# Performance work log

Hardware: AMD Instinct MI355X
Metric: run time of the kernel (lower is better)

The kernel has to match this reference:

```python
import jax, jax.numpy as jnp
import numpy as np

N_LAYERS, D_MODEL, H, D_K, D_V, D_FF, VOCAB = 6, 512, 8, 64, 64, 2048, 32000
B, S = 4, 512
NEG_INF = -jnp.inf


def positional_encoding(seq_len, d_model):
    # Faithful to the (buggy-vs-paper) source: angle = pos / 10000**(2*i/d_model),
    # sin for even i, cos for odd i (i is the raw channel index).
    pos = jnp.arange(seq_len, dtype=jnp.float32)[:, None]
    i = jnp.arange(d_model, dtype=jnp.float32)[None, :]
    angle = pos / jnp.power(10000.0, 2.0 * i / d_model)
    return jnp.where((jnp.arange(d_model) % 2 == 0)[None, :], jnp.sin(angle), jnp.cos(angle))


def layer_norm(x, g, b, eps=1e-5):
    mu = jnp.mean(x, -1, keepdims=True)
    var = jnp.mean((x - mu) ** 2, -1, keepdims=True)
    return (x - mu) * jax.lax.rsqrt(var + eps) * g + b


def mha(q_in, k_in, v_in, wq, wk, wv, wo, q_mask, k_mask, causal):
    # wq/wk: (H, D, D_K), wv: (H, D, D_V), wo: (H*D_V, D)
    q = jnp.einsum('bsd,hdk->bhsk', q_in, wq)
    k = jnp.einsum('btd,hdk->bhtk', k_in, wk)
    v = jnp.einsum('btd,hdk->bhtk', v_in, wv)
    scores = jnp.einsum('bhsk,bhtk->bhst', q, k) / jnp.sqrt(jnp.float32(D_K))
    allowed = q_mask[:, None, :, None] & k_mask[:, None, None, :]  # (B,1,S,T)
    if causal:
        sl, tl = q_in.shape[1], k_in.shape[1]
        allowed = allowed & (jnp.arange(tl)[None, :] <= jnp.arange(sl)[:, None])[None, None]
    scores = jnp.where(allowed, scores, NEG_INF)
    attn = jax.nn.softmax(scores, axis=-1)
    out = jnp.einsum('bhst,bhtk->bshk', attn, v)  # (B,S,H,D_V)
    out = out.reshape(out.shape[0], out.shape[1], H * D_V)
    return out @ wo


def ffn(x, w1, b1, w2, b2):
    return jax.nn.relu(x @ w1 + b1) @ w2 + b2


def setup_inputs() -> dict:
    key = jax.random.key(0)
    ks = iter(jax.random.split(key, 40))
    f = lambda shape, scale: (jax.random.normal(next(ks), shape, dtype=jnp.float32) * scale)
    inp = {
        'src_tokens': jax.random.randint(next(ks), (B, S), 0, VOCAB),
        'tgt_tokens': jax.random.randint(next(ks), (B, S), 0, VOCAB),
        'src_mask': jnp.ones((B, S), dtype=bool),
        'tgt_mask': jnp.ones((B, S), dtype=bool),
        'embed': f((VOCAB, D_MODEL), 0.02),
        'enc_wqkv': f((N_LAYERS, 3, H, D_MODEL, D_K), 0.04),
        'enc_wo': f((N_LAYERS, H * D_V, D_MODEL), 0.04),
        'enc_ff_w1': f((N_LAYERS, D_MODEL, D_FF), 0.02),
        'enc_ff_b1': jnp.zeros((N_LAYERS, D_FF), jnp.float32),
        'enc_ff_w2': f((N_LAYERS, D_FF, D_MODEL), 0.02),
        'enc_ff_b2': jnp.zeros((N_LAYERS, D_MODEL), jnp.float32),
        'enc_ln_g': jnp.ones((N_LAYERS, 2, D_MODEL), jnp.float32),
        'enc_ln_b': jnp.zeros((N_LAYERS, 2, D_MODEL), jnp.float32),
        'dec_wqkv1': f((N_LAYERS, 3, H, D_MODEL, D_K), 0.04),
        'dec_wo1': f((N_LAYERS, H * D_V, D_MODEL), 0.04),
        'dec_wqkv2': f((N_LAYERS, 3, H, D_MODEL, D_K), 0.04),
        'dec_wo2': f((N_LAYERS, H * D_V, D_MODEL), 0.04),
        'dec_ff_w1': f((N_LAYERS, D_MODEL, D_FF), 0.02),
        'dec_ff_b1': jnp.zeros((N_LAYERS, D_FF), jnp.float32),
        'dec_ff_w2': f((N_LAYERS, D_FF, D_MODEL), 0.02),
        'dec_ff_b2': jnp.zeros((N_LAYERS, D_MODEL), jnp.float32),
        'dec_ln_g': jnp.ones((N_LAYERS, 3, D_MODEL), jnp.float32),
        'dec_ln_b': jnp.zeros((N_LAYERS, 3, D_MODEL), jnp.float32),
        'out_w': f((D_MODEL, VOCAB), 0.02),
        'out_b': jnp.zeros((VOCAB,), jnp.float32),
    }
    return inp


def reference(src_tokens, tgt_tokens, src_mask, tgt_mask, embed,
              enc_wqkv, enc_wo, enc_ff_w1, enc_ff_b1, enc_ff_w2, enc_ff_b2, enc_ln_g, enc_ln_b,
              dec_wqkv1, dec_wo1, dec_wqkv2, dec_wo2, dec_ff_w1, dec_ff_b1, dec_ff_w2, dec_ff_b2,
              dec_ln_g, dec_ln_b, out_w, out_b):
    pe = positional_encoding(src_tokens.shape[1], D_MODEL)
    x = embed[src_tokens] + pe[None]
    for i in range(N_LAYERS):
        a = mha(x, x, x, enc_wqkv[i, 0], enc_wqkv[i, 1], enc_wqkv[i, 2], enc_wo[i], src_mask, src_mask, False)
        x = layer_norm(x + a, enc_ln_g[i, 0], enc_ln_b[i, 0])
        x = layer_norm(x + ffn(x, enc_ff_w1[i], enc_ff_b1[i], enc_ff_w2[i], enc_ff_b2[i]), enc_ln_g[i, 1], enc_ln_b[i, 1])
    pe_t = positional_encoding(tgt_tokens.shape[1], D_MODEL)
    y = embed[tgt_tokens] + pe_t[None]
    for i in range(N_LAYERS):
        a = mha(y, y, y, dec_wqkv1[i, 0], dec_wqkv1[i, 1], dec_wqkv1[i, 2], dec_wo1[i], tgt_mask, tgt_mask, True)
        y = layer_norm(y + a, dec_ln_g[i, 0], dec_ln_b[i, 0])
        a = mha(y, x, x, dec_wqkv2[i, 0], dec_wqkv2[i, 1], dec_wqkv2[i, 2], dec_wo2[i], tgt_mask, src_mask, False)
        y = layer_norm(y + a, dec_ln_g[i, 1], dec_ln_b[i, 1])
        y = layer_norm(y + ffn(y, dec_ff_w1[i], dec_ff_b1[i], dec_ff_w2[i], dec_ff_b2[i]), dec_ln_g[i, 2], dec_ln_b[i, 2])
    return y @ out_w + out_b
```

## Files before the change

### kernel.cpp

```cpp
#include <hip/hip_runtime.h>
#include <math.h>


typedef unsigned short u16;
typedef __attribute__((ext_vector_type(8))) short short8;
typedef __attribute__((ext_vector_type(4))) float f32x4;

__device__ __forceinline__ u16 f2bf(float f){
  unsigned u = __float_as_uint(f);
  return (u16)((u + 0x7fffu + ((u >> 16) & 1u)) >> 16);
}

#define GLDS16(gp, lp) __builtin_amdgcn_global_load_lds( \
    (const __attribute__((address_space(1))) unsigned int*)(const void*)(gp), \
    (__attribute__((address_space(3))) unsigned int*)(void*)(lp), 16, 0, 0)

__global__ __launch_bounds__(256) void embed_dual_kernel(
    const int* __restrict__ src, const int* __restrict__ tgt,
    const float* __restrict__ emb,
    float* __restrict__ xb, u16* __restrict__ xh,
    float* __restrict__ yb, u16* __restrict__ yh)
{
  int which = blockIdx.x >> 11;
  int row = blockIdx.x & 2047;
  int s = row & 511;
  int t = which ? tgt[row] : src[row];
  float* out = which ? yb : xb;
  u16*  outh = which ? yh : xh;
  #pragma unroll
  for (int j = 0; j < 2; j++){
    int d = threadIdx.x + 256*j;
    float ang = (float)s * powf(10000.0f, -2.0f*(float)d/512.0f);
    float pe = (d & 1) ? cosf(ang) : sinf(ang);
    float v = emb[(size_t)t*512 + d] + pe;
    out[(size_t)row*512 + d] = v;
    outh[(size_t)row*512 + d] = f2bf(v);
  }
}

struct WDesc { const float* W; unsigned long long gs, ds; u16* dst; int K; int nx; int end; };
struct WPack { WDesc d[6]; };

__device__ __forceinline__ void cast_body(const WPack& P, int nseg, int blk){
  __shared__ u16 T[64][65];
  int s = 0;
  while (s < nseg-1 && blk >= P.d[s].end) s++;
  WDesc D = P.d[s];
  int base = s ? P.d[s-1].end : 0;
  int lb = blk - base;
  int g = lb % D.nx, kt = lb / D.nx;
  int tid = threadIdx.x;
  const float* Wb = D.W + (size_t)g*D.gs + (size_t)kt*64*D.ds;
  #pragma unroll
  for (int i = 0; i < 16; i++){
    int li = tid + 256*i;
    int kk = li >> 6, c = li & 63;
    T[kk][c] = f2bf(Wb[(size_t)kk*D.ds + c]);
  }
  __syncthreads();
  #pragma unroll
  for (int i = 0; i < 16; i++){
    int lo = tid + 256*i;
    int c = lo >> 6, kk = lo & 63;
    D.dst[(size_t)(g*64 + c)*D.K + kt*64 + kk] = T[kk][c];
  }
}

__global__ __launch_bounds__(256) void wcast_multi(WPack P, int nseg){
  cast_body(P, nseg, blockIdx.x);
}

__device__ __forceinline__ void ln_body(
    float* __restrict__ x, const float* __restrict__ res,
    const float* __restrict__ g, const float* __restrict__ bt,
    u16* __restrict__ xh, int blk)
{
  int tid = threadIdx.x, lane = tid & 63, wv = tid >> 6;
  int row = blk*4 + wv;
  size_t base = (size_t)row*512;
  float v[8]; float sum = 0.f;
  #pragma unroll
  for (int j = 0; j < 8; j++){
    int d = lane + 64*j;
    v[j] = x[base + d] + res[base + d];
    sum += v[j];
  }
  #pragma unroll
  for (int o = 32; o; o >>= 1) sum += __shfl_xor(sum, o);
  float mu = sum * (1.0f/512.0f);
  float vs = 0.f;
  #pragma unroll
  for (int j = 0; j < 8; j++){ float dd = v[j] - mu; vs += dd*dd; }
  #pragma unroll
  for (int o = 32; o; o >>= 1) vs += __shfl_xor(vs, o);
  float rstd = rsqrtf(vs*(1.0f/512.0f) + 1e-5f);
  #pragma unroll
  for (int j = 0; j < 8; j++){
    int d = lane + 64*j;
    float ov = (v[j] - mu)*rstd*g[d] + bt[d];
    x[base + d] = ov;
    xh[base + d] = f2bf(ov);
  }
}

__global__ __launch_bounds__(256) void ln_cast_kernel(
    float* __restrict__ x, const float* __restrict__ res,
    const float* __restrict__ g, const float* __restrict__ bt,
    u16* __restrict__ xh, WPack P, int nseg)
{
  int bid = blockIdx.x;
  if (bid < 512){ ln_body(x, res, g, bt, xh, bid); return; }
  cast_body(P, nseg, bid - 512);
}

__global__ __launch_bounds__(256) void ln_kernel(
    float* __restrict__ x, const float* __restrict__ res,
    const float* __restrict__ g, const float* __restrict__ bt,
    u16* __restrict__ xh)
{
  ln_body(x, res, g, bt, xh, blockIdx.x);
}

__global__ __launch_bounds__(512) void flash_attn_kernel(
    const u16* __restrict__ qkv, const u16* __restrict__ vT,
    u16* __restrict__ ctx, int causal)
{
  __shared__ __align__(16) u16 lQ[64*64];
  __shared__ __align__(16) u16 lK[4][64*64];
  __shared__ __align__(16) u16 lV[4][64*64];
  __shared__ __align__(16) u16 lP[8][16*64];
  int tid = threadIdx.x, lane = tid & 63, w = tid >> 6;
  int g = w >> 2, wl = w & 3;
  int r16 = lane & 15, l4 = lane >> 4;
  int bh = blockIdx.x >> 3, qb = blockIdx.x & 7;
  int b = bh >> 3, h = bh & 7;
  const u16* qbase = qkv + (size_t)b*512*1536 + h*64;
  int sr = tid >> 3, sc = tid & 7;

  GLDS16(qbase + (size_t)(qb*64 + sr)*1536 + ((sc ^ (sr & 7))*8),
         lQ + (w << 6)*8);
  auto stageK = [&](int buf, int tt){
    GLDS16(qbase + 512 + (size_t)(tt*64 + sr)*1536 + ((sc ^ (sr & 7))*8),
           lK[buf] + (w << 6)*8);
  };
  auto stageV = [&](int buf, int tt){
    GLDS16(vT + ((size_t)bh*64 + sr)*512 + tt*64 + ((sc ^ (sr & 7))*8),
           lV[buf] + (w << 6)*8);
  };

  int ntl = causal ? (qb + 1) : 8;
  int nrounds = (ntl + 1) >> 1;
  stageK(0, 0); stageV(0, 0);
  if (ntl > 1){ stageK(1, 1); stageV(1, 1); }
  __syncthreads();

  short8 qa[2];
  #pragma unroll
  for (int kt = 0; kt < 2; kt++){
    int q = wl*16 + r16;
    qa[kt] = *(const short8*)&lQ[q*64 + (((kt*4 + l4) ^ (q & 7))*8)];
  }

  f32x4 o[4];
  float mrow[4], lrow[4];
  #pragma unroll
  for (int j = 0; j < 4; j++){ o[j] = (f32x4){0.f,0.f,0.f,0.f}; mrow[j] = -3e38f; lrow[j] = 0.f; }

  for (int rd = 0; rd < nrounds; rd++){
    if (rd > 0) __syncthreads();
    if (rd + 1 < nrounds){
      int base = ((rd + 1) & 1)*2;
      int t0 = 2*(rd + 1);
      stageK(base, t0); stageV(base, t0);
      if (t0 + 1 < ntl){ stageK(base + 1, t0 + 1); stageV(base + 1, t0 + 1); }
    }
    int tr = 2*rd + g;
    if (tr < ntl){
      int buf = (rd & 1)*2 + g;
      f32x4 s[4];
      #pragma unroll
      for (int ct = 0; ct < 4; ct++) s[ct] = (f32x4){0.f,0.f,0.f,0.f};
      __builtin_amdgcn_s_setprio(1);
      #pragma unroll
      for (int kt = 0; kt < 2; kt++){
        #pragma unroll
        for (int ct = 0; ct < 4; ct++){
          int trow = ct*16 + r16;
          short8 kb = *(const short8*)&lK[buf][trow*64 + (((kt*4 + l4) ^ (trow & 7))*8)];
          s[ct] = __builtin_amdgcn_mfma_f32_16x16x32_bf16(qa[kt], kb, s[ct], 0, 0, 0);
        }
      }
      __builtin_amdgcn_s_setprio(0);
      float p[4][4];
      #pragma unroll
      for (int ct = 0; ct < 4; ct++)
        #pragma unroll
        for (int r = 0; r < 4; r++){
          float v = s[ct][r] * 0.125f;
          if (causal && tr == qb && (ct*16 + r16) > (wl*16 + l4*4 + r)) v = -1e30f;
          p[ct][r] = v;
        }
      #pragma unroll
      for (int r = 0; r < 4; r++){
        float pm = fmaxf(fmaxf(p[0][r], p[1][r]), fmaxf(p[2][r], p[3][r]));
        #pragma unroll
        for (int off = 1; off < 16; off <<= 1) pm = fmaxf(pm, __shfl_xor(pm, off));
        float mn = fmaxf(mrow[r], pm);
        float scl = __expf(mrow[r] - mn);
        mrow[r] = mn;
        float rs = 0.f;
        #pragma unroll
        for (int ct = 0; ct < 4; ct++){ p[ct][r] = __expf(p[ct][r] - mn); rs += p[ct][r]; }
        #pragma unroll
        for (int off = 1; off < 16; off <<= 1) rs += __shfl_xor(rs, off);
        lrow[r] = lrow[r]*scl + rs;
        #pragma unroll
        for (int jf = 0; jf < 4; jf++) o[jf][r] *= scl;
      }
      u16* myP = &lP[w][0];
      #pragma unroll
      for (int ct = 0; ct < 4; ct++)
        #pragma unroll
        for (int r = 0; r < 4; r++){
          int q = l4*4 + r, t = ct*16 + r16;
          myP[q*64 + (((t >> 3) ^ (q & 7))*8) + (t & 7)] = f2bf(p[ct][r]);
        }
      __builtin_amdgcn_s_setprio(1);
      #pragma unroll
      for (int kt = 0; kt < 2; kt++){
        short8 pa = *(const short8*)&myP[r16*64 + (((kt*4 + l4) ^ (r16 & 7))*8)];
        #pragma unroll
        for (int jf = 0; jf < 4; jf++){
          int dr = jf*16 + r16;
          short8 vv = *(const short8*)&lV[buf][dr*64 + (((kt*4 + l4) ^ (dr & 7))*8)];
          o[jf] = __builtin_amdgcn_mfma_f32_16x16x32_bf16(pa, vv, o[jf], 0, 0, 0);
        }
      }
      __builtin_amdgcn_s_setprio(0);
    }
  }

  __syncthreads();
  float* mrg = (float*)&lK[0][0];
  if (w >= 4){
    float* p = mrg + ((size_t)(wl*64 + lane))*25;
    #pragma unroll
    for (int r = 0; r < 4; r++){ p[r] = mrow[r]; p[4 + r] = lrow[r]; }
    #pragma unroll
    for (int jf = 0; jf < 4; jf++)
      #pragma unroll
      for (int r = 0; r < 4; r++) p[8 + jf*4 + r] = o[jf][r];
  }
  __syncthreads();
  if (w < 4){
    float* p = mrg + ((size_t)(w*64 + lane))*25;
    #pragma unroll
    for (int r = 0; r < 4; r++){
      float m1 = p[r], l1 = p[4 + r];
      float M  = fmaxf(mrow[r], m1);
      float s0 = __expf(mrow[r] - M), s1 = __expf(m1 - M);
      float L  = lrow[r]*s0 + l1*s1;
      float inv = 1.0f / L;
      int q = qb*64 + w*16 + l4*4 + r;
      u16* dst = ctx + (size_t)(b*512 + q)*512 + h*64;
      #pragma unroll
      for (int jf = 0; jf < 4; jf++)
        dst[jf*16 + r16] = f2bf((o[jf][r]*s0 + p[8 + jf*4 + r]*s1) * inv);
    }
  }
}

template<int BM, int BN, int WM, int WN, int VOUT, int SWZ>
__global__ __launch_bounds__(WM*WN*64) void mfma_gemm(
    const u16* __restrict__ A, int lda,
    const u16* __restrict__ B, int ldb,
    void* __restrict__ C, int ldc, int cbf,
    const float* __restrict__ bias, int relu, int K, u16* __restrict__ vt)
{
  constexpr int NT  = WM*WN*64;
  constexpr int SM  = BM/WM, SN = BN/WN;
  constexpr int FM  = SM/16, FN = SN/16;
  constexpr int RPS = NT/8;
  constexpr int AG  = BM/RPS, BG = BN/RPS;
  __shared__ __align__(16) u16 lds[2][(BM+BN)*64];
  int bx, by;
  if constexpr (SWZ){
    int nwg = gridDim.x * gridDim.y;
    int lin = blockIdx.y * gridDim.x + blockIdx.x;
    int q = nwg >> 3, r = nwg & 7;
    int xcd = lin & 7, idx = lin >> 3;
    int wgid = (xcd < r ? xcd*(q+1) : r*(q+1) + (xcd-r)*q) + idx;
    bx = wgid / gridDim.y; by = wgid % gridDim.y;
  } else { bx = blockIdx.x; by = blockIdx.y; }
  int tid = threadIdx.x, lane = tid & 63, w = tid >> 6;
  int wm = w / WN, wn = w % WN;
  int r16 = lane & 15, l4 = lane >> 4;
  int sr = (w << 3) + (lane >> 3);
  int sc = lane & 7;
  int scs = sc ^ (sr & 7);
  const u16* Ab = A + (size_t)by*BM*lda + (size_t)sr*lda + scs*8;
  const u16* Bb = B + (size_t)bx*BN*ldb + (size_t)sr*ldb + scs*8;
  f32x4 acc[FM][FN];
  #pragma unroll
  for (int i = 0; i < FM; i++)
    #pragma unroll
    for (int j = 0; j < FN; j++)
      acc[i][j] = (f32x4){0.f, 0.f, 0.f, 0.f};

  auto stage = [&](int buf, int kt){
    #pragma unroll
    for (int s = 0; s < AG; s++)
      GLDS16(Ab + (size_t)(s*RPS)*lda + kt, &lds[buf][(s*RPS + (w << 3))*64]);
    #pragma unroll
    for (int s = 0; s < BG; s++)
      GLDS16(Bb + (size_t)(s*RPS)*ldb + kt, &lds[buf][(BM + s*RPS + (w << 3))*64]);
  };
  stage(0, 0);
  int nk = K >> 6, cur = 0;
  for (int kt = 0; kt < nk; kt++){
    __syncthreads();
    if (kt + 1 < nk) stage(cur ^ 1, (kt + 1) << 6);
    #pragma unroll
    for (int ks = 0; ks < 2; ks++){
      short8 av[FM], bv[FN];
      #pragma unroll
      for (int i = 0; i < FM; i++){
        int row = wm*SM + i*16 + r16;
        av[i] = *(const short8*)&lds[cur][row*64 + (((ks*4 + l4) ^ (row & 7))*8)];
      }
      #pragma unroll
      for (int j = 0; j < FN; j++){
        int row = wn*SN + j*16 + r16;
        bv[j] = *(const short8*)&lds[cur][(BM + row)*64 + (((ks*4 + l4) ^ (row & 7))*8)];
      }
      #pragma unroll
      for (int i = 0; i < FM; i++)
        #pragma unroll
        for (int j = 0; j < FN; j++)
          acc[i][j] = __builtin_amdgcn_mfma_f32_16x16x32_bf16(av[i], bv[j], acc[i][j], 0, 0, 0);
    }
    cur ^= 1;
  }

  if constexpr (VOUT){
    int nblk = bx * BN;
    if (nblk >= 1024){
      constexpr int TP = BM + 4;
      u16* T = &lds[0][0];
      __syncthreads();
      #pragma unroll
      for (int i = 0; i < FM; i++){
        int t0 = wm*SM + i*16 + l4*4;
        #pragma unroll
        for (int j = 0; j < FN; j++){
          int d = wn*SN + j*16 + r16;
          unsigned q01 = (unsigned)f2bf(acc[i][j][0]) | ((unsigned)f2bf(acc[i][j][1]) << 16);
          unsigned q23 = (unsigned)f2bf(acc[i][j][2]) | ((unsigned)f2bf(acc[i][j][3]) << 16);
          uint2 pk; pk.x = q01; pk.y = q23;
          *(uint2*)&T[d*TP + t0] = pk;
        }
      }
      __syncthreads();
      int h0 = (nblk - 1024) >> 6;
      int b = (by * BM) >> 9;
      int t0g = (by * BM) & 511;
      constexpr int U2PR = BM/4;
      constexpr int NIT = (BN*BM)/(NT*4);
      #pragma unroll
      for (int it = 0; it < NIT; it++){
        int idx = it*NT + tid;
        int d = idx / U2PR, tq = (idx % U2PR)*4;
        int hh = d >> 6, dd = d & 63;
        *(uint2*)&vt[((size_t)((b*8 + h0 + hh)*64 + dd))*512 + t0g + tq] =
            *(const uint2*)&T[d*TP + tq];
      }
      return;
    }
  }

  int m0 = by*BM + wm*SM, n0 = bx*BN + wn*SN;
  int r4 = l4*4;
  #pragma unroll
  for (int i = 0; i < FM; i++){
    #pragma unroll
    for (int j = 0; j < FN; j++){
      int col = n0 + j*16 + r16;
      float bi = bias ? bias[col] : 0.f;
      #pragma unroll
      for (int r = 0; r < 4; r++){
        int rowg = m0 + i*16 + r4 + r;
        float o = acc[i][j][r] + bi;
        if (relu) o = fmaxf(o, 0.f);
        if (cbf) ((u16*)C)[(size_t)rowg*ldc + col] = f2bf(o);
        else     ((float*)C)[(size_t)rowg*ldc + col] = o;
      }
    }
  }
}

__global__ __launch_bounds__(256) void xattn_qkv_gemm(
    const u16* __restrict__ Ay, const u16* __restrict__ Ax,
    const u16* __restrict__ Bt, u16* __restrict__ C, u16* __restrict__ vt)
{
  constexpr int BM=64, BN=64, WM=2, WN=2, NT=256;
  constexpr int SM=BM/WM, SN=BN/WN, FM=SM/16, FN=SN/16, RPS=NT/8;
  constexpr int AG=BM/RPS, BG=BN/RPS;
  __shared__ __align__(16) u16 lA[2][BM*64];
  __shared__ __align__(16) u16 lB[2][BN*64];
  int tid = threadIdx.x, lane = tid & 63, w = tid >> 6;
  int wm = w / WN, wn = w % WN;
  int r16 = lane & 15, l4 = lane >> 4;
  int sr = (w << 3) + (lane >> 3);
  int sc = lane & 7;
  int scs = sc ^ (sr & 7);
  int z = blockIdx.z;
  const u16* A = (z == 0) ? Ay : Ax;
  const u16* Ab = A + (size_t)blockIdx.y*BM*512 + (size_t)sr*512 + scs*8;
  const u16* Bb = Bt + (size_t)(z*512 + blockIdx.x*BN)*512 + (size_t)sr*512 + scs*8;
  f32x4 acc[FM][FN];
  #pragma unroll
  for (int i = 0; i < FM; i++)
    #pragma unroll
    for (int j = 0; j < FN; j++)
      acc[i][j] = (f32x4){0.f, 0.f, 0.f, 0.f};
  auto stage = [&](int buf, int kt){
    #pragma unroll
    for (int s = 0; s < AG; s++)
      GLDS16(Ab + (size_t)(s*RPS)*512 + kt, &lA[buf][(s*RPS + (w << 3))*64]);
    #pragma unroll
    for (int s = 0; s < BG; s++)
      GLDS16(Bb + (size_t)(s*RPS)*512 + kt, &lB[buf][(s*RPS + (w << 3))*64]);
  };
  stage(0, 0);
  int cur = 0;
  for (int kt = 0; kt < 8; kt++){
    __syncthreads();
    if (kt + 1 < 8) stage(cur ^ 1, (kt + 1) << 6);
    #pragma unroll
    for (int ks = 0; ks < 2; ks++){
      short8 av[FM], bv[FN];
      #pragma unroll
      for (int i = 0; i < FM; i++){
        int row = wm*SM + i*16 + r16;
        av[i] = *(const short8*)&lA[cur][row*64 + (((ks*4 + l4) ^ (row & 7))*8)];
      }
      #pragma unroll
      for (int j = 0; j < FN; j++){
        int row = wn*SN + j*16 + r16;
        bv[j] = *(const short8*)&lB[cur][row*64 + (((ks*4 + l4) ^ (row & 7))*8)];
      }
      #pragma unroll
      for (int i = 0; i < FM; i++)
        #pragma unroll
        for (int j = 0; j < FN; j++)
          acc[i][j] = __builtin_amdgcn_mfma_f32_16x16x32_bf16(av[i], bv[j], acc[i][j], 0, 0, 0);
    }
    cur ^= 1;
  }
  if (z == 2){
    constexpr int TP = BM + 4;
    u16* T = (u16*)&lA[0][0];
    __syncthreads();
    #pragma unroll
    for (int i = 0; i < FM; i++){
      int t0 = wm*SM + i*16 + l4*4;
      #pragma unroll
      for (int j = 0; j < FN; j++){
        int d = wn*SN + j*16 + r16;
        unsigned q01 = (unsigned)f2bf(acc[i][j][0]) | ((unsigned)f2bf(acc[i][j][1]) << 16);
        unsigned q23 = (unsigned)f2bf(acc[i][j][2]) | ((unsigned)f2bf(acc[i][j][3]) << 16);
        uint2 pk; pk.x = q01; pk.y = q23;
        *(uint2*)&T[d*TP + t0] = pk;
      }
    }
    __syncthreads();
    int h = blockIdx.x;
    int b = (blockIdx.y * BM) >> 9;
    int t0g = (blockIdx.y * BM) & 511;
    u16* dst = vt + (size_t)(b*8 + h)*64*512;
    #pragma unroll
    for (int it = 0; it < (BM*64)/(NT*4); it++){
      int idx = it*NT + tid;
      int d = idx >> 4, tq = (idx & 15)*4;
      *(uint2*)&dst[(size_t)d*512 + t0g + tq] = *(const uint2*)&T[d*TP + tq];
    }
    return;
  }
  int m0 = blockIdx.y*BM + wm*SM, n0 = z*512 + blockIdx.x*BN + wn*SN;
  int r4 = l4*4;
  #pragma unroll
  for (int i = 0; i < FM; i++)
    #pragma unroll
    for (int j = 0; j < FN; j++)
      #pragma unroll
      for (int r = 0; r < 4; r++){
        int rowg = m0 + i*16 + r4 + r;
        C[(size_t)rowg*1536 + n0 + j*16 + r16] = f2bf(acc[i][j][r]);
      }
}

extern "C" void kernel_launch(void* const* d_in, const int* in_sizes, int n_in,
                              void* d_out, int out_size, void* d_ws, size_t ws_size,
                              hipStream_t stream)
{
  (void)in_sizes; (void)n_in; (void)out_size; (void)ws_size;
  const int*   src_tok   = (const int*)  d_in[0];
  const int*   tgt_tok   = (const int*)  d_in[1];
  const float* emb       = (const float*)d_in[4];
  const float* enc_wqkv  = (const float*)d_in[5];
  const float* enc_wo    = (const float*)d_in[6];
  const float* enc_ff_w1 = (const float*)d_in[7];
  const float* enc_ff_b1 = (const float*)d_in[8];
  const float* enc_ff_w2 = (const float*)d_in[9];
  const float* enc_ff_b2 = (const float*)d_in[10];
  const float* enc_ln_g  = (const float*)d_in[11];
  const float* enc_ln_b  = (const float*)d_in[12];
  const float* dec_wqkv1 = (const float*)d_in[13];
  const float* dec_wo1   = (const float*)d_in[14];
  const float* dec_wqkv2 = (const float*)d_in[15];
  const float* dec_wo2   = (const float*)d_in[16];
  const float* dec_ff_w1 = (const float*)d_in[17];
  const float* dec_ff_b1 = (const float*)d_in[18];
  const float* dec_ff_w2 = (const float*)d_in[19];
  const float* dec_ff_b2 = (const float*)d_in[20];
  const float* dec_ln_g  = (const float*)d_in[21];
  const float* dec_ln_b  = (const float*)d_in[22];
  const float* out_w     = (const float*)d_in[23];
  const float* out_b     = (const float*)d_in[24];
  float* outp = (float*)d_out;

  const size_t MB = 1024*1024;
  char* wsb = (char*)d_ws;
  float* xb     = (float*)(wsb + 0*MB);
  u16*   sQKV2  = (u16*)  (wsb + 0*MB);
  u16*   sWO2   = (u16*)  (wsb + 1*MB + 512*1024);
  float* yb     = (float*)(wsb + 4*MB);
  u16*   xh     = (u16*)  (wsb + 8*MB);
  u16*   ctxb   = (u16*)  (wsb + 10*MB);
  u16*   yh     = (u16*)  (wsb + 12*MB);
  u16*   qkvb   = (u16*)  (wsb + 14*MB);
  u16*   vT     = (u16*)  (wsb + 20*MB);
  u16*   hid    = (u16*)  (wsb + 14*MB);
  u16*   sQKV   = (u16*)  (wsb + 22*MB);
  u16*   sWO    = (u16*)  (wsb + 23*MB + 512*1024);
  u16*   sFF1   = (u16*)  (wsb + 24*MB);
  u16*   sFF2   = (u16*)  (wsb + 26*MB);
  float* proj   = (float*)(wsb + 28*MB);
  u16*   wvbuf  = (u16*)  (wsb + 14*MB);

  auto g64 = [&](const u16* A,int lda,const u16* B,int ldb,void* C,int ldc,
                 int cbf,const float* bias,int relu,int M,int N,int K){
    mfma_gemm<64,64,2,2,0,0><<<dim3(N/64, M/64), 256, 0, stream>>>(
        A,lda,B,ldb,C,ldc,cbf,bias,relu,K,nullptr);
  };
  auto g128 = [&](const u16* A,int lda,const u16* B,int ldb,void* C,int ldc,
                  int cbf,const float* bias,int relu,int M,int N,int K){
    mfma_gemm<128,128,2,2,0,0><<<dim3(N/128, M/128), 256, 0, stream>>>(
        A,lda,B,ldb,C,ldc,cbf,bias,relu,K,nullptr);
  };
  auto gvocab = [&](const u16* A,const u16* B,void* C,int ldc,
                    const float* bias,int N){
    mfma_gemm<128,64,2,2,0,1><<<dim3(N/64, 16), 256, 0, stream>>>(
        A,512,B,512,C,ldc,0,bias,0,512,nullptr);
  };
  auto gqkv = [&](const u16* A,const u16* B,u16* C,u16* vt){
    mfma_gemm<128,128,2,2,1,0><<<dim3(12, 16), 256, 0, stream>>>(
        A,512,B,512,C,1536,1,nullptr,0,512,vt);
  };
  auto ln = [&](float* x, const float* g, const float* b, u16* oh){
    ln_kernel<<<512, 256, 0, stream>>>(x, proj, g, b, oh);
  };
  auto packof = [&](WDesc* segs, int n, int& tot){
    WPack P; tot = 0;
    for (int s = 0; s < n; s++){
      tot += segs[s].nx * (segs[s].K/64);
      segs[s].end = tot;
      P.d[s] = segs[s];
    }
    for (int s = n; s < 6; s++) P.d[s] = P.d[0];
    return P;
  };
  auto cast = [&](WDesc* segs, int n){
    int tot; WPack P = packof(segs, n, tot);
    wcast_multi<<<tot, 256, 0, stream>>>(P, n);
  };
  auto ln_cast = [&](float* x, const float* g, const float* b, u16* oh,
                     WDesc* segs, int n){
    int tot; WPack P = packof(segs, n, tot);
    ln_cast_kernel<<<512 + tot, 256, 0, stream>>>(x, proj, g, b, oh, P, n);
  };

  const size_t WQKV_L = (size_t)3*8*512*64;
  auto enc_segs = [&](int i, WDesc* s){
    s[0] = {enc_wqkv + i*WQKV_L,            32768, 64,   sQKV, 512,  24, 0};
    s[1] = {enc_wo   + (size_t)i*262144,    64,    512,  sWO,  512,  8,  0};
    s[2] = {enc_ff_w1+ (size_t)i*512*2048,  64,    2048, sFF1, 512,  32, 0};
    s[3] = {enc_ff_w2+ (size_t)i*2048*512,  64,    512,  sFF2, 2048, 8,  0};
  };
  auto dec_segs = [&](int i, WDesc* s){
    s[0] = {dec_wqkv1 + i*WQKV_L,           32768, 64,   sQKV,  512,  24, 0};
    s[1] = {dec_wo1   + (size_t)i*262144,   64,    512,  sWO,   512,  8,  0};
    s[2] = {dec_ff_w1 + (size_t)i*512*2048, 64,    2048, sFF1,  512,  32, 0};
    s[3] = {dec_ff_w2 + (size_t)i*2048*512, 64,    512,  sFF2,  2048, 8,  0};
    s[4] = {dec_wqkv2 + i*WQKV_L,           32768, 64,   sQKV2, 512,  24, 0};
    s[5] = {dec_wo2   + (size_t)i*262144,   64,    512,  sWO2,  512,  8,  0};
  };

  embed_dual_kernel<<<4096, 256, 0, stream>>>(src_tok, tgt_tok, emb, xb, xh, yb, yh);

  { WDesc s[4]; enc_segs(0, s); cast(s, 4); }
  for (int i = 0; i < 6; i++){
    gqkv(xh, sQKV, qkvb, vT);
    flash_attn_kernel<<<256, 512, 0, stream>>>(qkvb, vT, ctxb, 0);
    g64(ctxb, 512, sWO, 512, proj, 512, 0, nullptr, 0, 2048, 512, 512);
    ln(xb, enc_ln_g + i*1024, enc_ln_b + i*1024, xh);
    g128(xh, 512, sFF1, 512, hid, 2048, 1, enc_ff_b1 + i*2048, 1, 2048, 2048, 512);
    g64(hid, 2048, sFF2, 2048, proj, 512, 0, enc_ff_b2 + i*512, 0, 2048, 512, 2048);
    if (i < 5){
      WDesc s[4]; enc_segs(i+1, s);
      ln_cast(xb, enc_ln_g + i*1024 + 512, enc_ln_b + i*1024 + 512, xh, s, 4);
    } else {
      ln(xb, enc_ln_g + i*1024 + 512, enc_ln_b + i*1024 + 512, xh);
    }
  }

  { WDesc s[6]; dec_segs(0, s); cast(s, 6); }
  for (int i = 0; i < 6; i++){
    gqkv(yh, sQKV, qkvb, vT);
    flash_attn_kernel<<<256, 512, 0, stream>>>(qkvb, vT, ctxb, 1);
    g64(ctxb, 512, sWO, 512, proj, 512, 0, nullptr, 0, 2048, 512, 512);
    ln(yb, dec_ln_g + i*1536,        dec_ln_b + i*1536,        yh);
    xattn_qkv_gemm<<<dim3(8, 32, 3), 256, 0, stream>>>(yh, xh, sQKV2, qkvb, vT);
    flash_attn_kernel<<<256, 512, 0, stream>>>(qkvb, vT, ctxb, 0);
    g64(ctxb, 512, sWO2, 512, proj, 512, 0, nullptr, 0, 2048, 512, 512);
    ln(yb, dec_ln_g + i*1536 + 512,  dec_ln_b + i*1536 + 512,  yh);
    g128(yh, 512, sFF1, 512, hid, 2048, 1, dec_ff_b1 + i*2048, 1, 2048, 2048, 512);
    g64(hid, 2048, sFF2, 2048, proj, 512, 0, dec_ff_b2 + i*512, 0, 2048, 512, 2048);
    if (i < 5){
      WDesc s[6]; dec_segs(i+1, s);
      ln_cast(yb, dec_ln_g + i*1536 + 1024, dec_ln_b + i*1536 + 1024, yh, s, 6);
    } else {
      ln(yb, dec_ln_g + i*1536 + 1024, dec_ln_b + i*1536 + 1024, yh);
    }
  }

  for (int c = 0; c < 2; c++){
    int c0 = c*16000;
    WDesc seg[1] = {{out_w + c0, 64, 32000, wvbuf, 512, 250, 0}};
    cast(seg, 1);
    gvocab(yh, wvbuf, outp + c0, 32000, out_b + c0, 16000);
  }
}
```

Before: 1.343 ms.

## Add intra-block split-K with LDS reduction to MFMA GEMM

```diff
diff --git a/kernel.cpp b/kernel.cpp
--- a/kernel.cpp
+++ b/kernel.cpp
@@ -270,19 +270,21 @@
   }
 }
 
-template<int BM, int BN, int WM, int WN, int VOUT, int SWZ>
-__global__ __launch_bounds__(WM*WN*64) void mfma_gemm(
+template<int BM, int BN, int WM, int WN, int WK, int VOUT, int SWZ>
+__global__ __launch_bounds__(WM*WN*WK*64) void mfma_gemm(
     const u16* __restrict__ A, int lda,
     const u16* __restrict__ B, int ldb,
     void* __restrict__ C, int ldc, int cbf,
     const float* __restrict__ bias, int relu, int K, u16* __restrict__ vt)
 {
-  constexpr int NT  = WM*WN*64;
+  constexpr int NWC = WM*WN;
+  constexpr int NT  = NWC*WK*64;
+  constexpr int TPS = NWC*64;
   constexpr int SM  = BM/WM, SN = BN/WN;
   constexpr int FM  = SM/16, FN = SN/16;
-  constexpr int RPS = NT/8;
+  constexpr int RPS = TPS/8;
   constexpr int AG  = BM/RPS, BG = BN/RPS;
-  __shared__ __align__(16) u16 lds[2][(BM+BN)*64];
+  __shared__ __align__(16) u16 lds[2][WK][(BM+BN)*64];
   int bx, by;
   if constexpr (SWZ){
     int nwg = gridDim.x * gridDim.y;
@@ -293,13 +295,16 @@
     bx = wgid / gridDim.y; by = wgid % gridDim.y;
   } else { bx = blockIdx.x; by = blockIdx.y; }
   int tid = threadIdx.x, lane = tid & 63, w = tid >> 6;
-  int wm = w / WN, wn = w % WN;
+  int wk = w / NWC, wl = w % NWC;
+  int wm = wl / WN, wn = wl % WN;
   int r16 = lane & 15, l4 = lane >> 4;
-  int sr = (w << 3) + (lane >> 3);
-  int sc = lane & 7;
+  int stid = tid % TPS, slc = tid / TPS;
+  int ws = stid >> 6;
+  int sr = stid >> 3, sc = stid & 7;
   int scs = sc ^ (sr & 7);
-  const u16* Ab = A + (size_t)by*BM*lda + (size_t)sr*lda + scs*8;
-  const u16* Bb = B + (size_t)bx*BN*ldb + (size_t)sr*ldb + scs*8;
+  int kslc = K/WK;
+  const u16* Ab = A + (size_t)by*BM*lda + (size_t)sr*lda + scs*8 + (size_t)slc*kslc;
+  const u16* Bb = B + (size_t)bx*BN*ldb + (size_t)sr*ldb + scs*8 + (size_t)slc*kslc;
   f32x4 acc[FM][FN];
   #pragma unroll
   for (int i = 0; i < FM; i++)
@@ -310,13 +315,13 @@
   auto stage = [&](int buf, int kt){
     #pragma unroll
     for (int s = 0; s < AG; s++)
-      GLDS16(Ab + (size_t)(s*RPS)*lda + kt, &lds[buf][(s*RPS + (w << 3))*64]);
+      GLDS16(Ab + (size_t)(s*RPS)*lda + kt, &lds[buf][slc][(s*RPS + (ws << 3))*64]);
     #pragma unroll
     for (int s = 0; s < BG; s++)
-      GLDS16(Bb + (size_t)(s*RPS)*ldb + kt, &lds[buf][(BM + s*RPS + (w << 3))*64]);
+      GLDS16(Bb + (size_t)(s*RPS)*ldb + kt, &lds[buf][slc][(BM + s*RPS + (ws << 3))*64]);
   };
   stage(0, 0);
-  int nk = K >> 6, cur = 0;
+  int nk = kslc >> 6, cur = 0;
   for (int kt = 0; kt < nk; kt++){
     __syncthreads();
     if (kt + 1 < nk) stage(cur ^ 1, (kt + 1) << 6);
@@ -326,12 +331,12 @@
       #pragma unroll
       for (int i = 0; i < FM; i++){
         int row = wm*SM + i*16 + r16;
-        av[i] = *(const short8*)&lds[cur][row*64 + (((ks*4 + l4) ^ (row & 7))*8)];
+        av[i] = *(const short8*)&lds[cur][wk][row*64 + (((ks*4 + l4) ^ (row & 7))*8)];
       }
       #pragma unroll
       for (int j = 0; j < FN; j++){
         int row = wn*SN + j*16 + r16;
-        bv[j] = *(const short8*)&lds[cur][(BM + row)*64 + (((ks*4 + l4) ^ (row & 7))*8)];
+        bv[j] = *(const short8*)&lds[cur][wk][(BM + row)*64 + (((ks*4 + l4) ^ (row & 7))*8)];
       }
       #pragma unroll
       for (int i = 0; i < FM; i++)
@@ -340,24 +345,52 @@
           acc[i][j] = __builtin_amdgcn_mfma_f32_16x16x32_bf16(av[i], bv[j], acc[i][j], 0, 0, 0);
     }
     cur ^= 1;
+  }
+
+  if constexpr (WK == 2){
+    __syncthreads();
+    float* Mg = (float*)&lds[0][0][0];
+    if (wk == 1){
+      #pragma unroll
+      for (int i = 0; i < FM; i++)
+        #pragma unroll
+        for (int j = 0; j < FN; j++)
+          #pragma unroll
+          for (int r = 0; r < 4; r++)
+            Mg[(size_t)(wm*SM + i*16 + l4*4 + r)*(BN + 4) + wn*SN + j*16 + r16]
+                = acc[i][j][r];
+    }
+    __syncthreads();
+    if (wk == 0){
+      #pragma unroll
+      for (int i = 0; i < FM; i++)
+        #pragma unroll
+        for (int j = 0; j < FN; j++)
+          #pragma unroll
+          for (int r = 0; r < 4; r++)
+            acc[i][j][r] += Mg[(size_t)(wm*SM + i*16 + l4*4 + r)*(BN + 4)
+                               + wn*SN + j*16 + r16];
+    }
   }
 
   if constexpr (VOUT){
     int nblk = bx * BN;
     if (nblk >= 1024){
       constexpr int TP = BM + 4;
-      u16* T = &lds[0][0];
+      u16* T = &lds[0][0][0];
       __syncthreads();
-      #pragma unroll
-      for (int i = 0; i < FM; i++){
-        int t0 = wm*SM + i*16 + l4*4;
-        #pragma unroll
-        for (int j = 0; j < FN; j++){
-          int d = wn*SN + j*16 + r16;
-          unsigned q01 = (unsigned)f2bf(acc[i][j][0]) | ((unsigned)f2bf(acc[i][j][1]) << 16);
-          unsigned q23 = (unsigned)f2bf(acc[i][j][2]) | ((unsigned)f2bf(acc[i][j][3]) << 16);
-          uint2 pk; pk.x = q01; pk.y = q23;
-          *(uint2*)&T[d*TP + t0] = pk;
+      if (wk == 0){
+        #pragma unroll
+        for (int i = 0; i < FM; i++){
+          int t0 = wm*SM + i*16 + l4*4;
+          #pragma unroll
+          for (int j = 0; j < FN; j++){
+            int d = wn*SN + j*16 + r16;
+            unsigned q01 = (unsigned)f2bf(acc[i][j][0]) | ((unsigned)f2bf(acc[i][j][1]) << 16);
+            unsigned q23 = (unsigned)f2bf(acc[i][j][2]) | ((unsigned)f2bf(acc[i][j][3]) << 16);
+            uint2 pk; pk.x = q01; pk.y = q23;
+            *(uint2*)&T[d*TP + t0] = pk;
+          }
         }
       }
       __syncthreads();
@@ -378,6 +411,7 @@
     }
   }
 
+  if (wk != 0) return;
   int m0 = by*BM + wm*SM, n0 = bx*BN + wn*SN;
   int r4 = l4*4;
   #pragma unroll
@@ -550,21 +584,21 @@
 
   auto g64 = [&](const u16* A,int lda,const u16* B,int ldb,void* C,int ldc,
                  int cbf,const float* bias,int relu,int M,int N,int K){
-    mfma_gemm<64,64,2,2,0,0><<<dim3(N/64, M/64), 256, 0, stream>>>(
+    mfma_gemm<64,64,2,2,2,0,0><<<dim3(N/64, M/64), 512, 0, stream>>>(
         A,lda,B,ldb,C,ldc,cbf,bias,relu,K,nullptr);
   };
   auto g128 = [&](const u16* A,int lda,const u16* B,int ldb,void* C,int ldc,
                   int cbf,const float* bias,int relu,int M,int N,int K){
-    mfma_gemm<128,128,2,2,0,0><<<dim3(N/128, M/128), 256, 0, stream>>>(
+    mfma_gemm<128,128,2,2,2,0,0><<<dim3(N/128, M/128), 512, 0, stream>>>(
         A,lda,B,ldb,C,ldc,cbf,bias,relu,K,nullptr);
   };
   auto gvocab = [&](const u16* A,const u16* B,void* C,int ldc,
                     const float* bias,int N){
-    mfma_gemm<128,64,2,2,0,1><<<dim3(N/64, 16), 256, 0, stream>>>(
+    mfma_gemm<128,64,2,2,1,0,1><<<dim3(N/64, 16), 256, 0, stream>>>(
         A,512,B,512,C,ldc,0,bias,0,512,nullptr);
   };
   auto gqkv = [&](const u16* A,const u16* B,u16* C,u16* vt){
-    mfma_gemm<128,128,2,2,1,0><<<dim3(12, 16), 256, 0, stream>>>(
+    mfma_gemm<128,128,2,2,2,1,0><<<dim3(12, 16), 512, 0, stream>>>(
         A,512,B,512,C,1536,1,nullptr,0,512,vt);
   };
   auto ln = [&](float* x, const float* g, const float* b, u16* oh){
```

Result: faster. 1.298 ms, median of 2 (-3.3%).
